# Kernel tuning notes

Measured on AMD Instinct MI355X. Metric: run time of the kernel, lower is better.

The kernel has to match this reference:

```python
import jax, jax.numpy as jnp
import numpy as np

NW = 8            # qubits per circuit
DIM = 2 ** NW     # 256 state-vector amplitudes
ATTN_WIRES = [0, 1, 2, 3, 4, 5, 6, 7]
FFN_WIRES = [0, 1, 2, 2, 4, 5, 6, 7]   # faithful bug: input 3 -> wire 2, wire 3 never encoded

# PauliZ sign of wire w for basis state idx (wire 0 = most significant bit, torchquantum layout)
_bits = (np.arange(DIM)[None, :] >> (NW - 1 - np.arange(NW)[:, None])) & 1
SIGNS = jnp.asarray(1.0 - 2.0 * _bits, dtype=jnp.float32)  # (8, 256)


def _rx(state, theta, w):
    """Apply RX(theta) on wire w. state: (N, 256) complex64, theta: (N,) float."""
    a, b = 2 ** w, 2 ** (NW - 1 - w)
    s = state.reshape(-1, a, 2, b)
    c = jnp.cos(theta * 0.5).astype(jnp.complex64)[:, None, None]
    sn = jnp.sin(theta * 0.5).astype(jnp.complex64)[:, None, None]
    s0, s1 = s[:, :, 0, :], s[:, :, 1, :]
    n0 = c * s0 - 1j * sn * s1
    n1 = -1j * sn * s0 + c * s1
    return jnp.stack([n0, n1], axis=2).reshape(-1, DIM)


def _cnot(state, c, t):
    """CNOT with control c, target t on (N, 256) state."""
    s = state.reshape((-1,) + (2,) * NW)
    s = jnp.moveaxis(s, (1 + c, 1 + t), (1, 2))
    s = jnp.concatenate([s[:, :1], s[:, 1:, ::-1]], axis=1)  # flip target where control==1
    s = jnp.moveaxis(s, (1, 2), (1 + c, 1 + t))
    return s.reshape(-1, DIM)


def qlayer(angles, thetas, wires):
    """Encoder RX(angles) per wire map, trainable RX, CNOT ring, PauliZ expectations.
    angles: (N, 8); thetas: (8,). Returns (N, 8) float32."""
    n = angles.shape[0]
    state = jnp.zeros((n, DIM), jnp.complex64).at[:, 0].set(1.0)  # |0...0>
    for i, w in enumerate(wires):
        state = _rx(state, angles[:, i], w)
    for w in range(NW):
        state = _rx(state, jnp.broadcast_to(thetas[w], (n,)), w)
    for k in range(NW):
        state = _cnot(state, k, (k + 1) % NW)
    probs = jnp.abs(state) ** 2          # (N, 256)
    return probs @ SIGNS.T               # (N, 8)


def layernorm(x, w, b, eps=1e-5):
    m = x.mean(-1, keepdims=True)
    v = x.var(-1, keepdims=True)
    return (x - m) / jnp.sqrt(v + eps) * w + b


def setup_inputs() -> dict:
    key = jax.random.key(0)
    ks = jax.random.split(key, 8)
    B, T, E = 128, 512, 8
    return {
        "x": jax.random.normal(ks[0], (B, T, E), jnp.float32),
        "thetas_attn": jax.random.normal(ks[1], (8,), jnp.float32),
        "thetas_ffn": jax.random.normal(ks[2], (8,), jnp.float32),
        "W_in": jax.random.normal(ks[3], (8, 8), jnp.float32) * (1.0 / np.sqrt(8)),
        "b_in": jax.random.normal(ks[4], (8,), jnp.float32) * 0.02,
        "W_out": jax.random.normal(ks[5], (8, 8), jnp.float32) * (1.0 / np.sqrt(8)),
        "b_out": jax.random.normal(ks[6], (8,), jnp.float32) * 0.02,
        "ln1_w": jnp.ones((8,), jnp.float32),
        "ln1_b": jnp.zeros((8,), jnp.float32),
        "ln2_w": jnp.ones((8,), jnp.float32),
        "ln2_b": jnp.zeros((8,), jnp.float32),
    }


def reference(x, thetas_attn, thetas_ffn, W_in, b_in, W_out, b_out,
              ln1_w, ln1_b, ln2_w, ln2_b):
    B, T, E = x.shape
    H = 2
    dk = E // H
    flat = x.reshape(B * T, E)
    # Q, K, V are the same quantum layer on the same input -> identical tensors
    qkv = qlayer(flat, thetas_attn, ATTN_WIRES).reshape(B, T, E)
    h = qkv.reshape(B, T, H, dk).transpose(0, 2, 1, 3)           # (B, H, T, dk)
    scores = jnp.einsum('bhqd,bhkd->bhqk', h, h) / jnp.sqrt(jnp.float32(dk))
    w_attn = jax.nn.softmax(scores, axis=-1)
    ctx = jnp.einsum('bhqk,bhkd->bhqd', w_attn, h)
    ctx = ctx.transpose(0, 2, 1, 3).reshape(B, T, E)
    # quantum output projection of the attention result
    attn_out = qlayer(ctx.reshape(B * T, E), thetas_attn, ATTN_WIRES).reshape(B, T, E)
    x1 = layernorm(attn_out + x, ln1_w, ln1_b)                   # dropout identity (eval)
    # quantum feed-forward: linear_in -> circuit (input detached in torch) -> linear_out
    hq = x1 @ W_in.T + b_in
    q = qlayer(jax.lax.stop_gradient(hq.reshape(B * T, E)), thetas_ffn, FFN_WIRES)
    ff = q.reshape(B, T, E) @ W_out.T + b_out
    return layernorm(ff + x1, ln2_w, ln2_b)
```

## Files before the change

kernel.cpp:

```cpp
#include <hip/hip_runtime.h>


__device__ __forceinline__ void zprod8(const float z[8], float out[8]) {
    float p = z[0];
#pragma unroll
    for (int w = 1; w < 8; ++w) { p *= z[w]; out[w] = p; }
    float q = z[1];
#pragma unroll
    for (int w = 2; w < 8; ++w) q *= z[w];
    out[0] = q;
}

__global__ __launch_bounds__(512) void k_fused(const float* __restrict__ x,
                                               const float* __restrict__ tha,
                                               const float* __restrict__ thf,
                                               const float* __restrict__ Win,
                                               const float* __restrict__ bin,
                                               const float* __restrict__ Wout,
                                               const float* __restrict__ bout,
                                               const float* __restrict__ ln1w,
                                               const float* __restrict__ ln1b,
                                               const float* __restrict__ ln2w,
                                               const float* __restrict__ ln2b,
                                               float* __restrict__ out) {
    const int qhalf = blockIdx.x & 1;
    const int b     = blockIdx.x >> 1;
    const int tid   = threadIdx.x;
    const int h     = tid >> 8;
    const int r     = tid & 255;

    __shared__ float4 kvs[512][2];

    {
        const float4* xp = (const float4*)(x + ((size_t)b * 512 + tid) * 8);
        const float4 a  = xp[0];
        const float4 bb = xp[1];
        const float ang[8] = {a.x, a.y, a.z, a.w, bb.x, bb.y, bb.z, bb.w};
        float z[8], o[8];
#pragma unroll
        for (int w = 0; w < 8; ++w) z[w] = __cosf(ang[w] + tha[w]);
        zprod8(z, o);
        kvs[tid][0] = make_float4(o[0], o[1], o[2], o[3]);
        kvs[tid][1] = make_float4(o[4], o[5], o[6], o[7]);
    }
    __syncthreads();

    const int qrow = qhalf * 256 + r;
    float4 qv = kvs[qrow][h];
    const float sc = 0.5f * 1.44269504088896f;
    qv.x *= sc; qv.y *= sc; qv.z *= sc; qv.w *= sc;

    float  l   = 0.0f;
    float4 acc = make_float4(0.f, 0.f, 0.f, 0.f);
#pragma unroll 8
    for (int k = 0; k < 512; ++k) {
        const float4 kk = kvs[k][h];
        const float s = fmaf(qv.x, kk.x,
                        fmaf(qv.y, kk.y,
                        fmaf(qv.z, kk.z, qv.w * kk.w)));
        const float p = __builtin_amdgcn_exp2f(s);
        l += p;
        acc.x = fmaf(p, kk.x, acc.x);
        acc.y = fmaf(p, kk.y, acc.y);
        acc.z = fmaf(p, kk.z, acc.z);
        acc.w = fmaf(p, kk.w, acc.w);
    }
    const float inv = 1.0f / l;
    const float4 cvh = make_float4(acc.x * inv, acc.y * inv,
                                   acc.z * inv, acc.w * inv);

    __syncthreads();
    kvs[r][h] = cvh;
    __syncthreads();

    if (tid < 256) {
        const size_t t = (size_t)b * 512 + qhalf * 256 + tid;

        const float4 ca = kvs[tid][0], cb = kvs[tid][1];
        const float cv[8] = {ca.x, ca.y, ca.z, ca.w, cb.x, cb.y, cb.z, cb.w};

        const float4* xp = (const float4*)(x + t * 8);
        const float4 xa = xp[0], xb = xp[1];
        const float xv[8] = {xa.x, xa.y, xa.z, xa.w, xb.x, xb.y, xb.z, xb.w};

        float z[8], ao[8];
#pragma unroll
        for (int w = 0; w < 8; ++w) z[w] = __cosf(cv[w] + tha[w]);
        zprod8(z, ao);

        float y[8], m = 0.f;
#pragma unroll
        for (int i = 0; i < 8; ++i) { y[i] = ao[i] + xv[i]; m += y[i]; }
        m *= 0.125f;
        float v = 0.f;
#pragma unroll
        for (int i = 0; i < 8; ++i) { const float d = y[i] - m; v += d * d; }
        v *= 0.125f;
        const float rs = rsqrtf(v + 1e-5f);
        float x1[8];
#pragma unroll
        for (int i = 0; i < 8; ++i) x1[i] = (y[i] - m) * rs * ln1w[i] + ln1b[i];

        float hq[8];
#pragma unroll
        for (int i = 0; i < 8; ++i) {
            float s = bin[i];
#pragma unroll
            for (int j = 0; j < 8; ++j) s = fmaf(x1[j], Win[i * 8 + j], s);
            hq[i] = s;
        }

        float phi[8];
        phi[0] = hq[0] + thf[0];
        phi[1] = hq[1] + thf[1];
        phi[2] = hq[2] + hq[3] + thf[2];
        phi[3] = thf[3];
        phi[4] = hq[4] + thf[4];
        phi[5] = hq[5] + thf[5];
        phi[6] = hq[6] + thf[6];
        phi[7] = hq[7] + thf[7];
        float qq[8];
#pragma unroll
        for (int w = 0; w < 8; ++w) z[w] = __cosf(phi[w]);
        zprod8(z, qq);

        float y2[8], m2 = 0.f;
#pragma unroll
        for (int i = 0; i < 8; ++i) {
            float s = bout[i];
#pragma unroll
            for (int j = 0; j < 8; ++j) s = fmaf(qq[j], Wout[i * 8 + j], s);
            y2[i] = s + x1[i];
            m2 += y2[i];
        }
        m2 *= 0.125f;
        float v2 = 0.f;
#pragma unroll
        for (int i = 0; i < 8; ++i) { const float d = y2[i] - m2; v2 += d * d; }
        v2 *= 0.125f;
        const float r2 = rsqrtf(v2 + 1e-5f);

        float o[8];
#pragma unroll
        for (int i = 0; i < 8; ++i) o[i] = (y2[i] - m2) * r2 * ln2w[i] + ln2b[i];

        float4* op = (float4*)(out + t * 8);
        op[0] = make_float4(o[0], o[1], o[2], o[3]);
        op[1] = make_float4(o[4], o[5], o[6], o[7]);
    }
}

extern "C" void kernel_launch(void* const* d_in, const int* in_sizes, int n_in,
                              void* d_out, int out_size, void* d_ws, size_t ws_size,
                              hipStream_t stream) {
    const float* x    = (const float*)d_in[0];
    const float* tha  = (const float*)d_in[1];
    const float* thf  = (const float*)d_in[2];
    const float* Win  = (const float*)d_in[3];
    const float* bin  = (const float*)d_in[4];
    const float* Wout = (const float*)d_in[5];
    const float* bout = (const float*)d_in[6];
    const float* ln1w = (const float*)d_in[7];
    const float* ln1b = (const float*)d_in[8];
    const float* ln2w = (const float*)d_in[9];
    const float* ln2b = (const float*)d_in[10];
    float* out = (float*)d_out;

    k_fused<<<256, 512, 0, stream>>>(x, tha, thf, Win, bin, Wout, bout,
                                     ln1w, ln1b, ln2w, ln2b, out);
}
```

Measured before the change: 94.93 us.

## Interleave key pairs in LDS and use packed FP32 math in attention loop

Rearranges the shared-memory key/value storage so two consecutive keys' components sit side by side, then processes two keys per iteration with v_pk_fma/v_pk_mul/v_pk_add packed FP32 instructions. This halves the number of scalar VALU ops for the score dot product and the context accumulation. A separate context buffer replaces reuse of the key buffer, which removes one barrier. The risk is that the inline-asm packed ops limit compiler scheduling, and the exp2 still runs as scalar per element.

```diff
diff --git a/kernel.cpp b/kernel.cpp
--- a/kernel.cpp
+++ b/kernel.cpp
@@ -1,5 +1,23 @@
 #include <hip/hip_runtime.h>
 
+
+typedef float v2f __attribute__((ext_vector_type(2)));
+
+__device__ __forceinline__ v2f pk_fma(v2f a, v2f b, v2f c) {
+    v2f d;
+    asm("v_pk_fma_f32 %0, %1, %2, %3" : "=v"(d) : "v"(a), "v"(b), "v"(c));
+    return d;
+}
+__device__ __forceinline__ v2f pk_mul(v2f a, v2f b) {
+    v2f d;
+    asm("v_pk_mul_f32 %0, %1, %2" : "=v"(d) : "v"(a), "v"(b));
+    return d;
+}
+__device__ __forceinline__ v2f pk_add(v2f a, v2f b) {
+    v2f d;
+    asm("v_pk_add_f32 %0, %1, %2" : "=v"(d) : "v"(a), "v"(b));
+    return d;
+}
 
 __device__ __forceinline__ void zprod8(const float z[8], float out[8]) {
     float p = z[0];
@@ -29,7 +47,9 @@
     const int h     = tid >> 8;
     const int r     = tid & 255;
 
-    __shared__ float4 kvs[512][2];
+    __shared__ float4 A[2][256];
+    __shared__ float4 Bv[2][256];
+    __shared__ float4 ctxs[256][2];
 
     {
         const float4* xp = (const float4*)(x + ((size_t)b * 512 + tid) * 8);
@@ -40,43 +60,64 @@
 #pragma unroll
         for (int w = 0; w < 8; ++w) z[w] = __cosf(ang[w] + tha[w]);
         zprod8(z, o);
-        kvs[tid][0] = make_float4(o[0], o[1], o[2], o[3]);
-        kvs[tid][1] = make_float4(o[4], o[5], o[6], o[7]);
+        const int s   = tid >> 1;
+        const int par = tid & 1;
+        float* a0 = (float*)&A[0][s];
+        a0[par] = o[0]; a0[2 + par] = o[1];
+        float* b0 = (float*)&Bv[0][s];
+        b0[par] = o[2]; b0[2 + par] = o[3];
+        float* a1 = (float*)&A[1][s];
+        a1[par] = o[4]; a1[2 + par] = o[5];
+        float* b1 = (float*)&Bv[1][s];
+        b1[par] = o[6]; b1[2 + par] = o[7];
     }
     __syncthreads();
 
     const int qrow = qhalf * 256 + r;
-    float4 qv = kvs[qrow][h];
+    const float4 qa = A[h][qrow >> 1];
+    const float4 qb = Bv[h][qrow >> 1];
+    const int qp = qrow & 1;
     const float sc = 0.5f * 1.44269504088896f;
-    qv.x *= sc; qv.y *= sc; qv.z *= sc; qv.w *= sc;
-
-    float  l   = 0.0f;
-    float4 acc = make_float4(0.f, 0.f, 0.f, 0.f);
+    const float qx = (qp ? qa.y : qa.x) * sc;
+    const float qy = (qp ? qa.w : qa.z) * sc;
+    const float qz = (qp ? qb.y : qb.x) * sc;
+    const float qw = (qp ? qb.w : qb.z) * sc;
+    const v2f qx2 = {qx, qx}, qy2 = {qy, qy}, qz2 = {qz, qz}, qw2 = {qw, qw};
+
+    v2f l2  = {0.f, 0.f};
+    v2f ax2 = {0.f, 0.f}, ay2 = {0.f, 0.f}, az2 = {0.f, 0.f}, aw2 = {0.f, 0.f};
+    const float4* pA = A[h];
+    const float4* pB = Bv[h];
 #pragma unroll 8
-    for (int k = 0; k < 512; ++k) {
-        const float4 kk = kvs[k][h];
-        const float s = fmaf(qv.x, kk.x,
-                        fmaf(qv.y, kk.y,
-                        fmaf(qv.z, kk.z, qv.w * kk.w)));
-        const float p = __builtin_amdgcn_exp2f(s);
-        l += p;
-        acc.x = fmaf(p, kk.x, acc.x);
-        acc.y = fmaf(p, kk.y, acc.y);
-        acc.z = fmaf(p, kk.z, acc.z);
-        acc.w = fmaf(p, kk.w, acc.w);
+    for (int j = 0; j < 256; ++j) {
+        const float4 ab = pA[j];
+        const float4 cd = pB[j];
+        const v2f kx2 = {ab.x, ab.y}, ky2 = {ab.z, ab.w};
+        const v2f kz2 = {cd.x, cd.y}, kw2 = {cd.z, cd.w};
+        v2f s2 = pk_mul(qw2, kw2);
+        s2 = pk_fma(qz2, kz2, s2);
+        s2 = pk_fma(qy2, ky2, s2);
+        s2 = pk_fma(qx2, kx2, s2);
+        v2f p2;
+        p2.x = __builtin_amdgcn_exp2f(s2.x);
+        p2.y = __builtin_amdgcn_exp2f(s2.y);
+        l2  = pk_add(l2, p2);
+        ax2 = pk_fma(p2, kx2, ax2);
+        ay2 = pk_fma(p2, ky2, ay2);
+        az2 = pk_fma(p2, kz2, az2);
+        aw2 = pk_fma(p2, kw2, aw2);
     }
-    const float inv = 1.0f / l;
-    const float4 cvh = make_float4(acc.x * inv, acc.y * inv,
-                                   acc.z * inv, acc.w * inv);
-
-    __syncthreads();
-    kvs[r][h] = cvh;
+    const float inv = 1.0f / (l2.x + l2.y);
+    const float4 cvh = make_float4((ax2.x + ax2.y) * inv, (ay2.x + ay2.y) * inv,
+                                   (az2.x + az2.y) * inv, (aw2.x + aw2.y) * inv);
+
+    ctxs[r][h] = cvh;
     __syncthreads();
 
     if (tid < 256) {
         const size_t t = (size_t)b * 512 + qhalf * 256 + tid;
 
-        const float4 ca = kvs[tid][0], cb = kvs[tid][1];
+        const float4 ca = ctxs[tid][0], cb = ctxs[tid][1];
         const float cv[8] = {ca.x, ca.y, ca.z, ca.w, cb.x, cb.y, cb.z, cb.w};
 
         const float4* xp = (const float4*)(x + t * 8);
```

After: 93.27 us. No clear change (-1.7%).
